# Kernel optimization log

Hardware: AMD Instinct MI355X
Metric: run time of the kernel (lower is better)

The kernel has to match this reference:

```python
import jax, jax.numpy as jnp
import numpy as np

N_NODES = 50000
N_EDGES = 800000
DIMS = [64, 128, 128, 64]  # input_dim -> hidden_dims
OUT_DIM = 64
N_CLASSES = 10


def _linear_params(key, in_f, out_f):
    kw, kb = jax.random.split(key)
    bound = 1.0 / np.sqrt(in_f)
    W = jax.random.uniform(kw, (out_f, in_f), jnp.float32, -bound, bound)
    b = jax.random.uniform(kb, (out_f,), jnp.float32, -bound, bound)
    return W, b


def setup_inputs() -> dict:
    key = jax.random.key(0)
    ks = jax.random.split(key, 8)
    x = jax.random.normal(ks[0], (N_NODES, DIMS[0]), jnp.float32)
    edge_index = jax.random.randint(ks[1], (2, N_EDGES), 0, N_NODES, jnp.int32)
    W1, b1 = _linear_params(ks[2], DIMS[0], DIMS[1])
    W2, b2 = _linear_params(ks[3], DIMS[1], DIMS[2])
    W3, b3 = _linear_params(ks[4], DIMS[2], DIMS[3])
    Wp, bp = _linear_params(ks[5], DIMS[3], OUT_DIM)
    Wc, bc = _linear_params(ks[6], DIMS[3], N_CLASSES)
    return {"node_features": x, "edge_index": edge_index,
            "W1": W1, "b1": b1, "W2": W2, "b2": b2, "W3": W3, "b3": b3,
            "Wp": Wp, "bp": bp, "Wc": Wc, "bc": bc}


def _conv_layer(x, src, dst, W, b):
    # mean-aggregate neighbor features via segment_sum over destination nodes
    n = x.shape[0]
    agg = jax.ops.segment_sum(x[src], dst, num_segments=n)  # [N, F]
    deg = jax.ops.segment_sum(jnp.ones_like(dst, jnp.float32), dst, num_segments=n)
    deg = jnp.maximum(deg, 1.0)
    agg = agg / deg[:, None]
    return jax.nn.relu((agg + x) @ W.T + b)


def reference(node_features, edge_index, W1, b1, W2, b2, W3, b3, Wp, bp, Wc, bc):
    src, dst = edge_index[0], edge_index[1]
    x = node_features
    # dropout is identity in eval mode
    x = _conv_layer(x, src, dst, W1, b1)
    x = _conv_layer(x, src, dst, W2, b2)
    x = _conv_layer(x, src, dst, W3, b3)
    node_embeddings = x
    next_event = x @ Wp.T + bp
    event_classes = x @ Wc.T + bc
    return node_embeddings, next_event, event_classes
```

## Files before the change

kernel.cpp:

```cpp
#include <hip/hip_runtime.h>
#include <hip/hip_bf16.h>

typedef __attribute__((ext_vector_type(8))) short short8;
typedef __attribute__((ext_vector_type(4))) float floatx4;

__device__ __forceinline__ float bf_lo(unsigned int u) { return __uint_as_float(u << 16); }
__device__ __forceinline__ float bf_hi(unsigned int u) { return __uint_as_float(u & 0xffff0000u); }

__device__ __forceinline__ unsigned short f2bf_rne(float f) {
    unsigned u = __float_as_uint(f);
    unsigned rb = (u >> 16) & 1u;
    u += 0x7fffu + rb;
    return (unsigned short)(u >> 16);
}
__device__ __forceinline__ unsigned int pack_bf2(float x, float y) {
    return (unsigned int)f2bf_rne(x) | ((unsigned int)f2bf_rne(y) << 16);
}

__device__ __forceinline__ void acc4(unsigned long long v, float& f0, float& f1, float& f2, float& f3) {
    unsigned ua = (unsigned)v, ub = (unsigned)(v >> 32);
    f0 += bf_lo(ua); f1 += bf_hi(ua); f2 += bf_lo(ub); f3 += bf_hi(ub);
}


__global__ __launch_bounds__(256) void prep_kernel(const int* __restrict__ dst,
                                                   int* __restrict__ deg,
                                                   unsigned short* __restrict__ rnk,
                                                   int E, int nCnt,
                                                   const float* __restrict__ x,
                                                   const float* __restrict__ W1,
                                                   const float* __restrict__ W2,
                                                   const float* __restrict__ W3,
                                                   const float* __restrict__ Wp, const float* __restrict__ bp,
                                                   const float* __restrict__ Wc, const float* __restrict__ bc,
                                                   unsigned int* __restrict__ xb,
                                                   unsigned int* __restrict__ W1b,
                                                   unsigned int* __restrict__ W2b,
                                                   unsigned int* __restrict__ W3b,
                                                   unsigned int* __restrict__ Whb,
                                                   float* __restrict__ hbias,
                                                   int nx) {
    if ((int)blockIdx.x < nCnt) {
        const int chunk = (E + nCnt - 1) / nCnt;
        const int lo = blockIdx.x * chunk;
        const int hi = min(lo + chunk, E);
        for (int e = lo + threadIdx.x; e < hi; e += 256) {
            int r = atomicAdd(&deg[dst[e]], 1);
            rnk[e] = (unsigned short)r;
        }
        return;
    }
    int i = (blockIdx.x - nCnt) * 256 + threadIdx.x;
    const int T0 = nx;
    const int T1 = T0 + 4096;
    const int T2 = T1 + 8192;
    const int T3 = T2 + 4096;
    const int T4 = T3 + 2560;
    const int T5 = T4 + 80;
    if (i < T0) {
        float2 f = ((const float2*)x)[i];
        xb[i] = pack_bf2(f.x, f.y);
    } else if (i < T1) {
        float2 f = ((const float2*)W1)[i - T0];
        W1b[i - T0] = pack_bf2(f.x, f.y);
    } else if (i < T2) {
        float2 f = ((const float2*)W2)[i - T1];
        W2b[i - T1] = pack_bf2(f.x, f.y);
    } else if (i < T3) {
        float2 f = ((const float2*)W3)[i - T2];
        W3b[i - T2] = pack_bf2(f.x, f.y);
    } else if (i < T4) {
        int j = i - T3;
        int r = j >> 5, c = (j & 31) * 2;
        float v0 = 0.f, v1 = 0.f;
        if (r < 64)      { v0 = Wp[r * 64 + c]; v1 = Wp[r * 64 + c + 1]; }
        else if (r < 74) { v0 = Wc[(r - 64) * 64 + c]; v1 = Wc[(r - 64) * 64 + c + 1]; }
        Whb[j] = pack_bf2(v0, v1);
    } else if (i < T5) {
        int j = i - T4;
        float v = 0.f;
        if (j < 64)      v = bp[j];
        else if (j < 74) v = bc[j - 64];
        hbias[j] = v;
    }
}

__global__ __launch_bounds__(256) void scatter_kernel(const int* __restrict__ src,
                                                      const int* __restrict__ dst,
                                                      const unsigned short* __restrict__ rnk,
                                                      const int* __restrict__ offsets,
                                                      unsigned short* __restrict__ csr_src, int E) {
    const int stride = gridDim.x * 256;
    for (int i = blockIdx.x * 256 + threadIdx.x; i < E; i += stride) {
        int d = dst[i];
        csr_src[offsets[d] + rnk[i]] = (unsigned short)src[i];
    }
}


__global__ __launch_bounds__(256) void partial_sum_kernel(const int* __restrict__ deg,
                                                          int* __restrict__ partial, int n) {
    __shared__ int s[256];
    int t = threadIdx.x;
    int i = blockIdx.x * 256 + t;
    s[t] = (i < n) ? deg[i] : 0;
    __syncthreads();
    for (int off = 128; off > 0; off >>= 1) {
        if (t < off) s[t] += s[t + off];
        __syncthreads();
    }
    if (t == 0) partial[blockIdx.x] = s[0];
}

__global__ __launch_bounds__(256) void local_scan_kernel(const int* __restrict__ deg,
                                                         const int* __restrict__ partial,
                                                         int* __restrict__ offsets,
                                                         int nblocks, int n) {
    __shared__ int sp[256];
    __shared__ int s[256];
    int t = threadIdx.x;
    sp[t] = (t < nblocks) ? partial[t] : 0;
    __syncthreads();
    for (int off = 1; off < 256; off <<= 1) {
        int u = (t >= off) ? sp[t - off] : 0;
        __syncthreads();
        sp[t] += u;
        __syncthreads();
    }
    const int blockbase = (blockIdx.x == 0) ? 0 : sp[blockIdx.x - 1];
    if (blockIdx.x == 0 && t == 0) offsets[n] = sp[nblocks - 1];

    int i = blockIdx.x * 256 + t;
    int v = (i < n) ? deg[i] : 0;
    s[t] = v;
    __syncthreads();
    for (int off = 1; off < 256; off <<= 1) {
        int u = (t >= off) ? s[t - off] : 0;
        __syncthreads();
        s[t] += u;
        __syncthreads();
    }
    if (i < n) offsets[i] = blockbase + s[t] - v;
}


template <int F_IN, int F_OUT, int MODE>
__global__ __launch_bounds__(512) void fused_agg_gemm_kernel(
        const unsigned long long* __restrict__ xt,
        const int* __restrict__ offsets,
        const unsigned short* __restrict__ csr_src,
        const unsigned short* __restrict__ Wb,
        const float* __restrict__ bias,
        unsigned short* __restrict__ Yb,
        float* __restrict__ Yf,
        float* __restrict__ nev, float* __restrict__ cls,
        const unsigned short* __restrict__ Whb, const float* __restrict__ hbias,
        int n) {
    constexpr int KC   = F_IN / 32;
    constexpr int XSTR = F_IN / 4;
    constexpr int HSTR = F_IN + 8;
    __shared__ __align__(16) unsigned short Ht[32 * HSTR];
    __shared__ __align__(16) unsigned short Yt[(MODE == 3) ? 32 * 72 : 16];

    const int lane = threadIdx.x & 63;
    const int wv   = threadIdx.x >> 6;
    const int m0   = blockIdx.x * 32;

    if (F_IN == 64) {
        const int g   = lane >> 4;
        const int c   = lane & 15;
        const int row = wv * 4 + g;
        const int node = m0 + row;
        int ns = 0, ne = 0;
        if (node < n) { ns = offsets[node]; ne = offsets[node + 1]; }
        const int cnt = ne - ns;
        unsigned long long sv = (node < n) ? xt[(size_t)node * XSTR + c] : 0ull;

        int mc = cnt;
        mc = max(mc, __shfl(mc, lane ^ 16, 64));
        mc = max(mc, __shfl(mc, lane ^ 32, 64));

        float s0 = 0.f, s1 = 0.f, s2 = 0.f, s3 = 0.f;
        int ii0 = ns + c;
        if (cnt > 0) { if (ii0 >= ne) ii0 = ne - 1; } else ii0 = 0;
        int idx = (mc > 0) ? (int)csr_src[ii0] : 0;

        for (int base = 0; base < mc; base += 16) {
            int idxN = 0;
            if (base + 16 < mc) {
                int ii = ns + base + 16 + c;
                if (cnt > 0) { if (ii >= ne) ii = ne - 1; } else ii = 0;
                idxN = csr_src[ii];
            }
            unsigned long long v[16];
#pragma unroll
            for (int q = 0; q < 16; ++q) {
                int nb = __shfl(idx, g * 16 + q, 64);
                if (base + q < cnt) v[q] = xt[(size_t)nb * XSTR + c];
            }
#pragma unroll
            for (int q = 0; q < 16; ++q)
                if (base + q < cnt) acc4(v[q], s0, s1, s2, s3);
            idx = idxN;
        }
        float inv = 1.0f / fmaxf((float)cnt, 1.0f);
        unsigned ua = (unsigned)sv, ub = (unsigned)(sv >> 32);
        unsigned o0 = pack_bf2(s0 * inv + bf_lo(ua), s1 * inv + bf_hi(ua));
        unsigned o1 = pack_bf2(s2 * inv + bf_lo(ub), s3 * inv + bf_hi(ub));
        *(unsigned long long*)&Ht[row * HSTR + c * 4] =
            ((unsigned long long)o1 << 32) | o0;
    } else {
        const int g = lane >> 5;
        const int c = lane & 31;
        const int row0 = wv * 4 + g;
        const int row1 = wv * 4 + 2 + g;
        const int node0 = m0 + row0, node1 = m0 + row1;
        int ns0 = 0, ne0 = 0, ns1 = 0, ne1 = 0;
        if (node0 < n) { ns0 = offsets[node0]; ne0 = offsets[node0 + 1]; }
        if (node1 < n) { ns1 = offsets[node1]; ne1 = offsets[node1 + 1]; }
        const int cnt0 = ne0 - ns0, cnt1 = ne1 - ns1;
        unsigned long long sv0 = (node0 < n) ? xt[(size_t)node0 * XSTR + c] : 0ull;
        unsigned long long sv1 = (node1 < n) ? xt[(size_t)node1 * XSTR + c] : 0ull;
        int mc0 = max(cnt0, __shfl(cnt0, lane ^ 32, 64));
        int mc1 = max(cnt1, __shfl(cnt1, lane ^ 32, 64));
        int iiA = ns0 + (c & 15);
        if (cnt0 > 0) { if (iiA >= ne0) iiA = ne0 - 1; } else iiA = 0;
        int iiB = ns1 + (c & 15);
        if (cnt1 > 0) { if (iiB >= ne1) iiB = ne1 - 1; } else iiB = 0;
        int idx0 = (mc0 > 0) ? (int)csr_src[iiA] : 0;
        int idx1 = (mc1 > 0) ? (int)csr_src[iiB] : 0;

        {
            float s0 = 0.f, s1 = 0.f, s2 = 0.f, s3 = 0.f;
            int idx = idx0;
            for (int base = 0; base < mc0; base += 16) {
                int idxN = 0;
                if (base + 16 < mc0) {
                    int ii = ns0 + base + 16 + (c & 15);
                    if (cnt0 > 0) { if (ii >= ne0) ii = ne0 - 1; } else ii = 0;
                    idxN = csr_src[ii];
                }
                unsigned long long v[16];
#pragma unroll
                for (int q = 0; q < 16; ++q) {
                    int nb = __shfl(idx, g * 32 + q, 64);
                    if (base + q < cnt0) v[q] = xt[(size_t)nb * XSTR + c];
                }
#pragma unroll
                for (int q = 0; q < 16; ++q)
                    if (base + q < cnt0) acc4(v[q], s0, s1, s2, s3);
                idx = idxN;
            }
            float inv = 1.0f / fmaxf((float)cnt0, 1.0f);
            unsigned ua = (unsigned)sv0, ub = (unsigned)(sv0 >> 32);
            unsigned o0 = pack_bf2(s0 * inv + bf_lo(ua), s1 * inv + bf_hi(ua));
            unsigned o1 = pack_bf2(s2 * inv + bf_lo(ub), s3 * inv + bf_hi(ub));
            *(unsigned long long*)&Ht[row0 * HSTR + c * 4] =
                ((unsigned long long)o1 << 32) | o0;
        }
        {
            float s0 = 0.f, s1 = 0.f, s2 = 0.f, s3 = 0.f;
            int idx = idx1;
            for (int base = 0; base < mc1; base += 16) {
                int idxN = 0;
                if (base + 16 < mc1) {
                    int ii = ns1 + base + 16 + (c & 15);
                    if (cnt1 > 0) { if (ii >= ne1) ii = ne1 - 1; } else ii = 0;
                    idxN = csr_src[ii];
                }
                unsigned long long v[16];
#pragma unroll
                for (int q = 0; q < 16; ++q) {
                    int nb = __shfl(idx, g * 32 + q, 64);
                    if (base + q < cnt1) v[q] = xt[(size_t)nb * XSTR + c];
                }
#pragma unroll
                for (int q = 0; q < 16; ++q)
                    if (base + q < cnt1) acc4(v[q], s0, s1, s2, s3);
                idx = idxN;
            }
            float inv = 1.0f / fmaxf((float)cnt1, 1.0f);
            unsigned ua = (unsigned)sv1, ub = (unsigned)(sv1 >> 32);
            unsigned o0 = pack_bf2(s0 * inv + bf_lo(ua), s1 * inv + bf_hi(ua));
            unsigned o1 = pack_bf2(s2 * inv + bf_lo(ub), s3 * inv + bf_hi(ub));
            *(unsigned long long*)&Ht[row1 * HSTR + c * 4] =
                ((unsigned long long)o1 << 32) | o0;
        }
    }
    __syncthreads();

    const int quad = lane >> 4;
    const int r16  = lane & 15;

    if (MODE == 0) {
        const int rowg = wv & 1;
        const int cg0  = (wv >> 1) * 2;
        short8 a[KC];
#pragma unroll
        for (int c = 0; c < KC; ++c)
            a[c] = *(const short8*)&Ht[(16 * rowg + r16) * HSTR + 32 * c + quad * 8];

        floatx4 acc[2];
#pragma unroll
        for (int j = 0; j < 2; ++j)
#pragma unroll
            for (int r = 0; r < 4; ++r) acc[j][r] = 0.f;

#pragma unroll
        for (int j = 0; j < 2; ++j)
#pragma unroll
            for (int c = 0; c < KC; ++c) {
                short8 b = *(const short8*)&Wb[(size_t)(16 * (cg0 + j) + r16) * F_IN + 32 * c + quad * 8];
                acc[j] = __builtin_amdgcn_mfma_f32_16x16x32_bf16(a[c], b, acc[j], 0, 0, 0);
            }

#pragma unroll
        for (int r = 0; r < 4; ++r) {
            const int mm = m0 + 16 * rowg + quad * 4 + r;
            if (mm >= n) continue;
#pragma unroll
            for (int j = 0; j < 2; ++j) {
                const int o = 16 * (cg0 + j) + r16;
                Yb[(size_t)mm * F_OUT + o] = f2bf_rne(fmaxf(acc[j][r] + bias[o], 0.f));
            }
        }
    } else {
        const int rowg = wv & 1;
        const int cg   = wv >> 1;
        short8 a[KC];
#pragma unroll
        for (int c = 0; c < KC; ++c)
            a[c] = *(const short8*)&Ht[(16 * rowg + r16) * HSTR + 32 * c + quad * 8];

        floatx4 acc;
#pragma unroll
        for (int r = 0; r < 4; ++r) acc[r] = 0.f;

#pragma unroll
        for (int c = 0; c < KC; ++c) {
            short8 b = *(const short8*)&Wb[(size_t)(16 * cg + r16) * F_IN + 32 * c + quad * 8];
            acc = __builtin_amdgcn_mfma_f32_16x16x32_bf16(a[c], b, acc, 0, 0, 0);
        }

#pragma unroll
        for (int r = 0; r < 4; ++r) {
            const int lr = 16 * rowg + quad * 4 + r;
            const int mm = m0 + lr;
            const int o  = 16 * cg + r16;
            if (mm < n) {
                float v = fmaxf(acc[r] + bias[o], 0.f);
                Yf[(size_t)mm * 64 + o] = v;
                Yt[lr * 72 + o] = f2bf_rne(v);
            } else {
                Yt[lr * 72 + o] = 0;
            }
        }
        __syncthreads();

        for (int t = wv; t < 10; t += 8) {
            const int rg  = t & 1;
            const int cg2 = t >> 1;
            short8 a2[2];
#pragma unroll
            for (int c = 0; c < 2; ++c)
                a2[c] = *(const short8*)&Yt[(16 * rg + r16) * 72 + 32 * c + quad * 8];

            floatx4 acc2;
#pragma unroll
            for (int r = 0; r < 4; ++r) acc2[r] = 0.f;

#pragma unroll
            for (int c = 0; c < 2; ++c) {
                short8 b = *(const short8*)&Whb[(size_t)(16 * cg2 + r16) * 64 + 32 * c + quad * 8];
                acc2 = __builtin_amdgcn_mfma_f32_16x16x32_bf16(a2[c], b, acc2, 0, 0, 0);
            }

#pragma unroll
            for (int r = 0; r < 4; ++r) {
                const int mm = m0 + 16 * rg + quad * 4 + r;
                if (mm >= n) continue;
                const int o = 16 * cg2 + r16;
                float v = acc2[r] + hbias[o];
                if (o < 64)      nev[(size_t)mm * 64 + o] = v;
                else if (o < 74) cls[(size_t)mm * 10 + (o - 64)] = v;
            }
        }
    }
}


extern "C" void kernel_launch(void* const* d_in, const int* in_sizes, int n_in,
                              void* d_out, int out_size, void* d_ws, size_t ws_size,
                              hipStream_t stream) {
    const float* x  = (const float*)d_in[0];
    const int*   ei = (const int*)d_in[1];
    const float* W1 = (const float*)d_in[2];
    const float* b1 = (const float*)d_in[3];
    const float* W2 = (const float*)d_in[4];
    const float* b2 = (const float*)d_in[5];
    const float* W3 = (const float*)d_in[6];
    const float* b3 = (const float*)d_in[7];
    const float* Wp = (const float*)d_in[8];
    const float* bp = (const float*)d_in[9];
    const float* Wc = (const float*)d_in[10];
    const float* bc = (const float*)d_in[11];

    const int n = in_sizes[0] / 64;
    const int E = in_sizes[1] / 2;
    const int* src = ei;
    const int* dst = ei + E;

    const int nScanBlocks = (n + 255) / 256;

    int* deg       = (int*)d_ws;
    int* offsets   = deg + n;
    int* partial   = offsets + (n + 1);
    unsigned short* rnk     = (unsigned short*)(partial + 256);
    unsigned short* csr_src = rnk + E;
    uintptr_t p = (uintptr_t)(csr_src + E);
    p = (p + 255) & ~(uintptr_t)255;
    unsigned int* Hb  = (unsigned int*)p;
    unsigned int* Yb  = Hb + (size_t)n * 64;
    unsigned int* xb  = Yb + (size_t)n * 64;
    unsigned int* W1b = xb + (size_t)n * 32;
    unsigned int* W2b = W1b + 4096;
    unsigned int* W3b = W2b + 8192;
    unsigned int* Whb = W3b + 4096;
    float* hbias = (float*)(Whb + 2560);

    float* out_emb = (float*)d_out;
    float* out_nev = out_emb + (size_t)n * 64;
    float* out_cls = out_nev + (size_t)n * 64;

    hipMemsetAsync(deg, 0, (size_t)n * sizeof(int), stream);

    const int nCnt = 256;
    const int convTotal = n * 32 + 4096 + 8192 + 4096 + 2560 + 80;
    const int convBlocks = (convTotal + 255) / 256;
    prep_kernel<<<nCnt + convBlocks, 256, 0, stream>>>(
        dst, deg, rnk, E, nCnt,
        x, W1, W2, W3, Wp, bp, Wc, bc, xb, W1b, W2b, W3b, Whb, hbias, n * 32);

    partial_sum_kernel<<<nScanBlocks, 256, 0, stream>>>(deg, partial, n);
    local_scan_kernel<<<nScanBlocks, 256, 0, stream>>>(deg, partial, offsets, nScanBlocks, n);

    scatter_kernel<<<1024, 256, 0, stream>>>(src, dst, rnk, offsets, csr_src, E);

    const int gF = (n + 31) / 32;

    fused_agg_gemm_kernel<64, 128, 0><<<gF, 512, 0, stream>>>(
        (const unsigned long long*)xb, offsets, csr_src,
        (const unsigned short*)W1b, b1, (unsigned short*)Hb,
        nullptr, nullptr, nullptr, nullptr, nullptr, n);

    fused_agg_gemm_kernel<128, 128, 0><<<gF, 512, 0, stream>>>(
        (const unsigned long long*)Hb, offsets, csr_src,
        (const unsigned short*)W2b, b2, (unsigned short*)Yb,
        nullptr, nullptr, nullptr, nullptr, nullptr, n);

    fused_agg_gemm_kernel<128, 64, 3><<<gF, 512, 0, stream>>>(
        (const unsigned long long*)Yb, offsets, csr_src,
        (const unsigned short*)W3b, b3, nullptr,
        out_emb, out_nev, out_cls, (const unsigned short*)Whb, hbias, n);
}
```

Before: 254.2 us.

## Build CSR with two-pass bucketed radix sort instead of global atomics

```diff
diff --git a/kernel.cpp b/kernel.cpp
--- a/kernel.cpp
+++ b/kernel.cpp
@@ -3,6 +3,9 @@
 
 typedef __attribute__((ext_vector_type(8))) short short8;
 typedef __attribute__((ext_vector_type(4))) float floatx4;
+
+#define NB   196
+#define NBLK 256
 
 __device__ __forceinline__ float bf_lo(unsigned int u) { return __uint_as_float(u << 16); }
 __device__ __forceinline__ float bf_hi(unsigned int u) { return __uint_as_float(u & 0xffff0000u); }
@@ -24,9 +27,8 @@
 
 
 __global__ __launch_bounds__(256) void prep_kernel(const int* __restrict__ dst,
-                                                   int* __restrict__ deg,
-                                                   unsigned short* __restrict__ rnk,
-                                                   int E, int nCnt,
+                                                   int* __restrict__ blockcnt,
+                                                   int E,
                                                    const float* __restrict__ x,
                                                    const float* __restrict__ W1,
                                                    const float* __restrict__ W2,
@@ -40,17 +42,21 @@
                                                    unsigned int* __restrict__ Whb,
                                                    float* __restrict__ hbias,
                                                    int nx) {
-    if ((int)blockIdx.x < nCnt) {
-        const int chunk = (E + nCnt - 1) / nCnt;
+    if ((int)blockIdx.x < NBLK) {
+        __shared__ int hist[NB];
+        for (int i = threadIdx.x; i < NB; i += 256) hist[i] = 0;
+        __syncthreads();
+        const int chunk = (E + NBLK - 1) / NBLK;
         const int lo = blockIdx.x * chunk;
         const int hi = min(lo + chunk, E);
-        for (int e = lo + threadIdx.x; e < hi; e += 256) {
-            int r = atomicAdd(&deg[dst[e]], 1);
-            rnk[e] = (unsigned short)r;
-        }
+        for (int e = lo + threadIdx.x; e < hi; e += 256)
+            atomicAdd(&hist[dst[e] >> 8], 1);
+        __syncthreads();
+        for (int i = threadIdx.x; i < NB; i += 256)
+            blockcnt[i * NBLK + blockIdx.x] = hist[i];
         return;
     }
-    int i = (blockIdx.x - nCnt) * 256 + threadIdx.x;
+    int i = (blockIdx.x - NBLK) * 256 + threadIdx.x;
     const int T0 = nx;
     const int T1 = T0 + 4096;
     const int T2 = T1 + 8192;
@@ -85,25 +91,13 @@
     }
 }
 
-__global__ __launch_bounds__(256) void scatter_kernel(const int* __restrict__ src,
-                                                      const int* __restrict__ dst,
-                                                      const unsigned short* __restrict__ rnk,
-                                                      const int* __restrict__ offsets,
-                                                      unsigned short* __restrict__ csr_src, int E) {
-    const int stride = gridDim.x * 256;
-    for (int i = blockIdx.x * 256 + threadIdx.x; i < E; i += stride) {
-        int d = dst[i];
-        csr_src[offsets[d] + rnk[i]] = (unsigned short)src[i];
-    }
-}
-
-
-__global__ __launch_bounds__(256) void partial_sum_kernel(const int* __restrict__ deg,
+
+__global__ __launch_bounds__(256) void partial_sum_kernel(const int* __restrict__ v,
                                                           int* __restrict__ partial, int n) {
     __shared__ int s[256];
     int t = threadIdx.x;
     int i = blockIdx.x * 256 + t;
-    s[t] = (i < n) ? deg[i] : 0;
+    s[t] = (i < n) ? v[i] : 0;
     __syncthreads();
     for (int off = 128; off > 0; off >>= 1) {
         if (t < off) s[t] += s[t + off];
@@ -112,9 +106,9 @@
     if (t == 0) partial[blockIdx.x] = s[0];
 }
 
-__global__ __launch_bounds__(256) void local_scan_kernel(const int* __restrict__ deg,
+__global__ __launch_bounds__(256) void local_scan_kernel(const int* __restrict__ v,
                                                          const int* __restrict__ partial,
-                                                         int* __restrict__ offsets,
+                                                         int* __restrict__ base,
                                                          int nblocks, int n) {
     __shared__ int sp[256];
     __shared__ int s[256];
@@ -128,11 +122,11 @@
         __syncthreads();
     }
     const int blockbase = (blockIdx.x == 0) ? 0 : sp[blockIdx.x - 1];
-    if (blockIdx.x == 0 && t == 0) offsets[n] = sp[nblocks - 1];
+    if (blockIdx.x == 0 && t == 0) base[n] = sp[nblocks - 1];
 
     int i = blockIdx.x * 256 + t;
-    int v = (i < n) ? deg[i] : 0;
-    s[t] = v;
+    int w = (i < n) ? v[i] : 0;
+    s[t] = w;
     __syncthreads();
     for (int off = 1; off < 256; off <<= 1) {
         int u = (t >= off) ? s[t - off] : 0;
@@ -140,7 +134,74 @@
         s[t] += u;
         __syncthreads();
     }
-    if (i < n) offsets[i] = blockbase + s[t] - v;
+    if (i < n) base[i] = blockbase + s[t] - w;
+}
+
+
+__global__ __launch_bounds__(256) void binC_kernel(const int* __restrict__ src,
+                                                   const int* __restrict__ dst,
+                                                   const int* __restrict__ base,
+                                                   unsigned int* __restrict__ pairs, int E) {
+    __shared__ int bbase[NB];
+    __shared__ int cur[NB];
+    for (int i = threadIdx.x; i < NB; i += 256) {
+        bbase[i] = base[i * NBLK + blockIdx.x];
+        cur[i] = 0;
+    }
+    __syncthreads();
+    const int chunk = (E + NBLK - 1) / NBLK;
+    const int lo = blockIdx.x * chunk;
+    const int hi = min(lo + chunk, E);
+    for (int e = lo + threadIdx.x; e < hi; e += 256) {
+        int d = dst[e];
+        int b = d >> 8;
+        int r = atomicAdd(&cur[b], 1);
+        pairs[bbase[b] + r] = ((unsigned)d << 16) | (unsigned)src[e];
+    }
+}
+
+
+__global__ __launch_bounds__(256) void bucketD_kernel(const unsigned int* __restrict__ pairs,
+                                                      const int* __restrict__ base,
+                                                      int* __restrict__ offsets,
+                                                      unsigned short* __restrict__ csr_src,
+                                                      int E, int n) {
+    __shared__ int cnt[256];
+    __shared__ int loc[256];
+    const int b = blockIdx.x;
+    const int start = base[b * NBLK];
+    const int end   = base[(b + 1) * NBLK];
+    const int t = threadIdx.x;
+
+    cnt[t] = 0;
+    __syncthreads();
+    for (int i = start + t; i < end; i += 256)
+        atomicAdd(&cnt[(pairs[i] >> 16) & 255], 1);
+    __syncthreads();
+
+    loc[t] = cnt[t];
+    __syncthreads();
+    for (int off = 1; off < 256; off <<= 1) {
+        int u = (t >= off) ? loc[t - off] : 0;
+        __syncthreads();
+        loc[t] += u;
+        __syncthreads();
+    }
+    const int excl = (t == 0) ? 0 : loc[t - 1];
+
+    const int d = (b << 8) + t;
+    if (d < n) offsets[d] = start + excl;
+    if (b == 0 && t == 0) offsets[n] = E;
+
+    __syncthreads();
+    cnt[t] = excl;
+    __syncthreads();
+    for (int i = start + t; i < end; i += 256) {
+        unsigned pr = pairs[i];
+        int j = (pr >> 16) & 255;
+        int p = atomicAdd(&cnt[j], 1);
+        csr_src[start + p] = (unsigned short)(pr & 0xffffu);
+    }
 }
 
 
@@ -410,13 +471,15 @@
     const int* src = ei;
     const int* dst = ei + E;
 
-    const int nScanBlocks = (n + 255) / 256;
-
-    int* deg       = (int*)d_ws;
-    int* offsets   = deg + n;
-    int* partial   = offsets + (n + 1);
-    unsigned short* rnk     = (unsigned short*)(partial + 256);
-    unsigned short* csr_src = rnk + E;
+    const int items = NB * NBLK;
+    const int nScan = (items + 255) / 256;
+
+    int* blockcnt = (int*)d_ws;
+    int* base     = blockcnt + items;
+    int* partial  = base + items + 1;
+    int* offsets  = partial + 256;
+    unsigned int*   pairs   = (unsigned int*)(offsets + n + 1);
+    unsigned short* csr_src = (unsigned short*)(pairs + E);
     uintptr_t p = (uintptr_t)(csr_src + E);
     p = (p + 255) & ~(uintptr_t)255;
     unsigned int* Hb  = (unsigned int*)p;
@@ -432,19 +495,17 @@
     float* out_nev = out_emb + (size_t)n * 64;
     float* out_cls = out_nev + (size_t)n * 64;
 
-    hipMemsetAsync(deg, 0, (size_t)n * sizeof(int), stream);
-
-    const int nCnt = 256;
     const int convTotal = n * 32 + 4096 + 8192 + 4096 + 2560 + 80;
     const int convBlocks = (convTotal + 255) / 256;
-    prep_kernel<<<nCnt + convBlocks, 256, 0, stream>>>(
-        dst, deg, rnk, E, nCnt,
+    prep_kernel<<<NBLK + convBlocks, 256, 0, stream>>>(
+        dst, blockcnt, E,
         x, W1, W2, W3, Wp, bp, Wc, bc, xb, W1b, W2b, W3b, Whb, hbias, n * 32);
 
-    partial_sum_kernel<<<nScanBlocks, 256, 0, stream>>>(deg, partial, n);
-    local_scan_kernel<<<nScanBlocks, 256, 0, stream>>>(deg, partial, offsets, nScanBlocks, n);
-
-    scatter_kernel<<<1024, 256, 0, stream>>>(src, dst, rnk, offsets, csr_src, E);
+    partial_sum_kernel<<<nScan, 256, 0, stream>>>(blockcnt, partial, items);
+    local_scan_kernel<<<nScan, 256, 0, stream>>>(blockcnt, partial, base, nScan, items);
+
+    binC_kernel<<<NBLK, 256, 0, stream>>>(src, dst, base, pairs, E);
+    bucketD_kernel<<<NB, 256, 0, stream>>>(pairs, base, offsets, csr_src, E, n);
 
     const int gF = (n + 31) / 32;
 
```

Result: faster. 230.2 us, median of 2 (-9.4%).
